# Kernel optimization log

Hardware: AMD Instinct MI355X
Metric: run time of the kernel (lower is better)

## Reference

```python
import jax, jax.numpy as jnp
import numpy as np

B, T, N_EMBD = 4, 2048, 1024
N_EXP, TOP_K = 8, 2
EPS = 1e-9
EVAL_CAPACITY_FACTOR = 2.0
MIN_CAPACITY = 4
# eval-mode capacity: min(group_size, int(group_size * cap_factor / n_exp)), floored at min_capacity
CAPACITY = max(min(T, int(T * EVAL_CAPACITY_FACTOR / N_EXP)), MIN_CAPACITY)  # 512
THRESHOLD = np.array([EPS, 0.2], dtype=np.float32)  # threshold_eval buffer: [eps, *thresholds]


def setup_inputs() -> dict:
    key = jax.random.key(0)
    k1, k2, k3 = jax.random.split(key, 3)
    x = jax.random.normal(k1, (B, T, N_EMBD), dtype=jnp.float32)
    w_g = jax.random.normal(k2, (N_EXP, N_EMBD), dtype=jnp.float32) * 0.02
    probs = jax.random.uniform(k3, (TOP_K, B, T), dtype=jnp.float32)
    return {"x": x, "w_g": w_g, "probs": probs}


def reference(x, w_g, probs):
    # gate logits and softmax gates
    gate_logits = jnp.einsum('btd,ed->bte', x, w_g)          # [B,T,E]
    raw_gates = jax.nn.softmax(gate_logits, axis=-1)
    top_v, top_i = jax.lax.top_k(raw_gates, TOP_K)           # [B,T,k]
    gates = jnp.transpose(top_v, (2, 0, 1))                  # [k,B,T]
    gate_idx = jnp.transpose(top_i, (2, 0, 1))               # [k,B,T]
    one_hot_gate = jax.nn.one_hot(gate_idx, N_EXP, dtype=jnp.float32)  # [k,B,T,E]

    # renormalize top-k gates
    denom = jnp.clip(jnp.sum(gates, axis=0, keepdims=True), EPS, None)
    gates = gates / denom

    # stochastic thresholding (top-1 always routes)
    thr = jnp.asarray(THRESHOLD)[:, None, None]              # [k,1,1]
    should_route = probs < gates / jnp.clip(thr, EPS, None)
    should_route = should_route.at[0].set(True)
    mask = one_hot_gate * should_route[..., None].astype(jnp.float32)  # [k,B,T,E]

    # exclusive cumsum over tokens (dim T)
    mask_cumsum = jnp.cumsum(mask, axis=-2) - mask           # [k,B,T,E]

    masks, positions = [], []
    prev = jnp.zeros((B, 1, N_EXP), dtype=jnp.float32)
    cap_f = float(CAPACITY)
    for n in range(TOP_K):  # small fixed loop over routing ranks
        pos = (mask_cumsum[n] + prev) * mask[n]              # [B,T,E]
        m_n = mask[n] * (pos < cap_f).astype(jnp.float32)    # capacity drop
        prev = jnp.sum(m_n, axis=1, keepdims=True) + prev
        masks.append(m_n)
        positions.append(jnp.sum(pos, axis=-1))              # [B,T]
    mask = jnp.stack(masks)                                  # [k,B,T,E]
    positions = jnp.stack(positions)                         # [k,B,T]

    mask_flat = jnp.sum(mask, axis=-1)                       # [k,B,T] in {0,1}
    gates = gates * mask_flat

    # position one-hot; out-of-range positions map to all-zero rows (== safe_one_hot + slice)
    pos_oh = jax.nn.one_hot(positions.astype(jnp.int32), CAPACITY, dtype=jnp.float32)  # [k,B,T,C]

    # combine tensor: sum over k of gates * mask_flat * one_hot(expert) x one_hot(position)
    combine = jnp.einsum('kbt,kbte,kbtc->btec', gates * mask_flat, one_hot_gate, pos_oh)  # [B,T,E,C]

    dispatch_hard = (combine > 0).astype(combine.dtype)
    # straight-through dispatch tensor
    dispatch = dispatch_hard + combine - jax.lax.stop_gradient(combine)
    return dispatch, combine
```

## Files before the change

### kernel.cpp

```cpp
#include <hip/hip_runtime.h>

#define BB 4
#define TT 2048
#define DD 1024
#define EE 8
#define CAP 512
#define NTOK (BB*TT)
#define OUT_HALF ((size_t)NTOK * EE * CAP)

__global__ __launch_bounds__(256) void gate_zero_kernel(
    const float* __restrict__ x, const float* __restrict__ w,
    const float* __restrict__ probs,
    int* __restrict__ e0, int* __restrict__ e1, int* __restrict__ r1,
    float* __restrict__ v0, float* __restrict__ v1,
    float4* __restrict__ out4)
{
    size_t zbase = (size_t)blockIdx.x * 8192 + threadIdx.x;
    float4 z = make_float4(0.f, 0.f, 0.f, 0.f);
    #pragma unroll
    for (int i = 0; i < 32; ++i) out4[zbase + (size_t)i * 256] = z;

    const int wave = threadIdx.x >> 6;
    const int lane = threadIdx.x & 63;
    const int token = blockIdx.x * 4 + wave;
    const float* xt = x + (size_t)token * DD;

    float acc[EE];
    #pragma unroll
    for (int e = 0; e < EE; ++e) acc[e] = 0.f;

    #pragma unroll 4
    for (int i = 0; i < DD / 64; ++i) {
        float xv = xt[i * 64 + lane];
        #pragma unroll
        for (int e = 0; e < EE; ++e)
            acc[e] = fmaf(xv, w[e * DD + i * 64 + lane], acc[e]);
    }
    #pragma unroll
    for (int e = 0; e < EE; ++e) {
        #pragma unroll
        for (int off = 32; off > 0; off >>= 1)
            acc[e] += __shfl_xor(acc[e], off, 64);
    }

    if (lane == 0) {
        float mx = acc[0];
        #pragma unroll
        for (int e = 1; e < EE; ++e) mx = fmaxf(mx, acc[e]);
        float ex[EE]; float Z = 0.f;
        #pragma unroll
        for (int e = 0; e < EE; ++e) { ex[e] = expf(acc[e] - mx); Z += ex[e]; }
        int i0 = 0;
        #pragma unroll
        for (int e = 1; e < EE; ++e) if (ex[e] > ex[i0]) i0 = e;
        int i1 = (i0 == 0) ? 1 : 0;
        #pragma unroll
        for (int e = 0; e < EE; ++e) if (e != i0 && ex[e] > ex[i1]) i1 = e;
        float t0 = ex[i0] / Z, t1 = ex[i1] / Z;
        float den = fmaxf(t0 + t1, 1e-9f);
        float g0 = t0 / den, g1 = t1 / den;
        float p1 = probs[NTOK + token];
        int route = (p1 < g1 / 0.2f) ? 1 : 0;
        e0[token] = i0; e1[token] = i1; r1[token] = route;
        v0[token] = g0; v1[token] = g1;
    }
}

__global__ __launch_bounds__(1024) void scan_scatter_kernel(
    const int* __restrict__ e0, const int* __restrict__ e1, const int* __restrict__ r1,
    const float* __restrict__ v0, const float* __restrict__ v1,
    float* __restrict__ dispatch, float* __restrict__ combine)
{
    const int b = blockIdx.x;
    const int tid = threadIdx.x;
    const int wave = tid >> 6;
    const int lane = tid & 63;

    __shared__ int cnt[16][EE];
    __shared__ int off[16][EE];
    __shared__ int base[EE];

    if (tid < EE) base[tid] = 0;
    __syncthreads();

    for (int k = 0; k < 2; ++k) {
        for (int chunk = 0; chunk < 2; ++chunk) {
            const int t = chunk * 1024 + tid;
            const int gidx = b * TT + t;
            int e; float g; bool active;
            if (k == 0) { e = e0[gidx]; g = v0[gidx]; active = true; }
            else        { e = e1[gidx]; g = v1[gidx]; active = (r1[gidx] != 0); }

            if (tid < 16 * EE) cnt[tid >> 3][tid & 7] = 0;
            __syncthreads();

            unsigned long long act = __ballot(active);
            unsigned long long m = act;
            #pragma unroll
            for (int bit = 0; bit < 3; ++bit) {
                unsigned long long bm = __ballot((e >> bit) & 1);
                m &= ((e >> bit) & 1) ? bm : ~bm;
            }
            int rank = __popcll(m & ((1ull << lane) - 1ull));
            if (active && rank == 0) cnt[wave][e] = __popcll(m);
            __syncthreads();

            if (tid < EE) {
                int run = base[tid];
                #pragma unroll
                for (int w = 0; w < 16; ++w) { off[w][tid] = run; run += cnt[w][tid]; }
                base[tid] = run;
            }
            __syncthreads();

            if (active) {
                int pos = off[wave][e] + rank;
                if (pos < CAP) {
                    size_t oi = (((size_t)gidx) * EE + e) * CAP + pos;
                    dispatch[oi] = 1.0f;
                    combine[oi]  = g;
                }
            }
            __syncthreads();
        }
        if (k == 0) {
            if (tid < EE) base[tid] = min(base[tid], CAP);
            __syncthreads();
        }
    }
}

extern "C" void kernel_launch(void* const* d_in, const int* in_sizes, int n_in,
                              void* d_out, int out_size, void* d_ws, size_t ws_size,
                              hipStream_t stream) {
    const float* x     = (const float*)d_in[0];
    const float* w     = (const float*)d_in[1];
    const float* probs = (const float*)d_in[2];
    float* out = (float*)d_out;

    int*   e0 = (int*)d_ws;
    int*   e1 = e0 + NTOK;
    int*   r1 = e1 + NTOK;
    float* v0 = (float*)(r1 + NTOK);
    float* v1 = v0 + NTOK;

    gate_zero_kernel<<<2048, 256, 0, stream>>>(x, w, probs, e0, e1, r1, v0, v1,
                                               (float4*)out);
    scan_scatter_kernel<<<4, 1024, 0, stream>>>(e0, e1, r1, v0, v1,
                                                out, out + OUT_HALF);
}
```

Measured before the change: 82.53 us.

## Replace zero-fill plus scatter with a single dense fill of dispatch and combine

The output zeroing is moved out of the gate kernel. The scan kernel now only records each token's flat target slot (expert*CAP+pos, or -1 if dropped) in place of the expert indices. A new per-token kernel then writes every dispatch and combine element once, with the correct value at the target slots, so the separate sparse scatter after zeroing goes away. The cost is that the gate matmul's read of x no longer overlaps with the output writes, and there is one more kernel launch.

```diff
diff --git a/kernel.cpp b/kernel.cpp
--- a/kernel.cpp
+++ b/kernel.cpp
@@ -8,18 +8,12 @@
 #define NTOK (BB*TT)
 #define OUT_HALF ((size_t)NTOK * EE * CAP)
 
-__global__ __launch_bounds__(256) void gate_zero_kernel(
+__global__ __launch_bounds__(256) void gate_kernel(
     const float* __restrict__ x, const float* __restrict__ w,
     const float* __restrict__ probs,
     int* __restrict__ e0, int* __restrict__ e1, int* __restrict__ r1,
-    float* __restrict__ v0, float* __restrict__ v1,
-    float4* __restrict__ out4)
+    float* __restrict__ v0, float* __restrict__ v1)
 {
-    size_t zbase = (size_t)blockIdx.x * 8192 + threadIdx.x;
-    float4 z = make_float4(0.f, 0.f, 0.f, 0.f);
-    #pragma unroll
-    for (int i = 0; i < 32; ++i) out4[zbase + (size_t)i * 256] = z;
-
     const int wave = threadIdx.x >> 6;
     const int lane = threadIdx.x & 63;
     const int token = blockIdx.x * 4 + wave;
@@ -66,10 +60,9 @@
     }
 }
 
-__global__ __launch_bounds__(1024) void scan_scatter_kernel(
-    const int* __restrict__ e0, const int* __restrict__ e1, const int* __restrict__ r1,
-    const float* __restrict__ v0, const float* __restrict__ v1,
-    float* __restrict__ dispatch, float* __restrict__ combine)
+__global__ __launch_bounds__(1024) void scan_kernel(
+    int* __restrict__ e0, int* __restrict__ e1, const int* __restrict__ r1,
+    const float* __restrict__ v0, const float* __restrict__ v1)
 {
     const int b = blockIdx.x;
     const int tid = threadIdx.x;
@@ -87,9 +80,9 @@
         for (int chunk = 0; chunk < 2; ++chunk) {
             const int t = chunk * 1024 + tid;
             const int gidx = b * TT + t;
-            int e; float g; bool active;
-            if (k == 0) { e = e0[gidx]; g = v0[gidx]; active = true; }
-            else        { e = e1[gidx]; g = v1[gidx]; active = (r1[gidx] != 0); }
+            int e; bool active;
+            if (k == 0) { e = e0[gidx]; active = true; }
+            else        { e = e1[gidx]; active = (r1[gidx] != 0); }
 
             if (tid < 16 * EE) cnt[tid >> 3][tid & 7] = 0;
             __syncthreads();
@@ -113,20 +106,50 @@
             }
             __syncthreads();
 
+            int tgt = -1;
             if (active) {
                 int pos = off[wave][e] + rank;
-                if (pos < CAP) {
-                    size_t oi = (((size_t)gidx) * EE + e) * CAP + pos;
-                    dispatch[oi] = 1.0f;
-                    combine[oi]  = g;
-                }
+                if (pos < CAP) tgt = e * CAP + pos;
             }
+            if (k == 0) e0[gidx] = tgt; else e1[gidx] = tgt;
             __syncthreads();
         }
         if (k == 0) {
             if (tid < EE) base[tid] = min(base[tid], CAP);
             __syncthreads();
         }
+    }
+}
+
+__global__ __launch_bounds__(256) void fill_scatter_kernel(
+    const int* __restrict__ t0, const int* __restrict__ t1,
+    const float* __restrict__ v0, const float* __restrict__ v1,
+    float4* __restrict__ out)
+{
+    const int token = blockIdx.x;
+    const int tid = threadIdx.x;
+    const int a0 = t0[token];
+    const int a1 = t1[token];
+    const float g0 = v0[token];
+    const float g1 = v1[token];
+
+    float4* drow = out + (size_t)token * 1024;
+    float4* crow = out + (OUT_HALF / 4) + (size_t)token * 1024;
+
+    #pragma unroll
+    for (int i = 0; i < 4; ++i) {
+        const int f = i * 1024 + tid * 4;
+        float4 d, c;
+        d.x = (f + 0 == a0 || f + 0 == a1) ? 1.f : 0.f;
+        d.y = (f + 1 == a0 || f + 1 == a1) ? 1.f : 0.f;
+        d.z = (f + 2 == a0 || f + 2 == a1) ? 1.f : 0.f;
+        d.w = (f + 3 == a0 || f + 3 == a1) ? 1.f : 0.f;
+        c.x = (f + 0 == a0) ? g0 : ((f + 0 == a1) ? g1 : 0.f);
+        c.y = (f + 1 == a0) ? g0 : ((f + 1 == a1) ? g1 : 0.f);
+        c.z = (f + 2 == a0) ? g0 : ((f + 2 == a1) ? g1 : 0.f);
+        c.w = (f + 3 == a0) ? g0 : ((f + 3 == a1) ? g1 : 0.f);
+        drow[i * 256 + tid] = d;
+        crow[i * 256 + tid] = c;
     }
 }
 
@@ -144,8 +167,7 @@
     float* v0 = (float*)(r1 + NTOK);
     float* v1 = v0 + NTOK;
 
-    gate_zero_kernel<<<2048, 256, 0, stream>>>(x, w, probs, e0, e1, r1, v0, v1,
-                                               (float4*)out);
-    scan_scatter_kernel<<<4, 1024, 0, stream>>>(e0, e1, r1, v0, v1,
-                                                out, out + OUT_HALF);
+    gate_kernel<<<2048, 256, 0, stream>>>(x, w, probs, e0, e1, r1, v0, v1);
+    scan_kernel<<<4, 1024, 0, stream>>>(e0, e1, r1, v0, v1);
+    fill_scatter_kernel<<<8192, 256, 0, stream>>>(e0, e1, v0, v1, (float4*)out);
 }
```

Result: faster. 68.19 us (-17.4%).
